# Kernel tuning notes

Hardware: AMD Instinct MI355X
Metric: run time of the kernel (lower is better)

The kernel has to match this reference:

```python
import jax, jax.numpy as jnp
import numpy as np

D = 256; R = 2; K = 32
N = 32768; NE = 1_000_000; NT = 65_536
BETA_MAX = 5.0; GRAD_CLIP = 1.0; STATE_CLIP = 10.0
DAMP = 0.9999  # update_damping=1.0 clamped to 1-1e-4
EPS = 1e-5


def _xavier(key, din, dout, gain=0.5):
    lim = gain * np.sqrt(6.0 / (din + dout))
    return jax.random.uniform(key, (din, dout), jnp.float32, -lim, lim)


def setup_inputs() -> dict:
    key = jax.random.key(0)
    ks = jax.random.split(key, 16)
    inv_sp1 = float(np.log(np.expm1(1.0)))  # inverse softplus of 1.0
    return {
        "X": jax.random.normal(ks[0], (N, D), jnp.float32),
        "c_2": jax.random.randint(ks[1], (NE,), 0, N, jnp.int32),
        "u_2": jax.random.randint(ks[2], (NE,), 0, N, jnp.int32),
        "c_3": jax.random.randint(ks[3], (NT,), 0, N, jnp.int32),
        "u_3": jax.random.randint(ks[4], (NT,), 0, N, jnp.int32),
        "v_3": jax.random.randint(ks[5], (NT,), 0, N, jnp.int32),
        "t_tau": jax.random.randint(ks[6], (NT,), 0, 2, jnp.int32),
        "step_size": jnp.float32(0.1),
        "ln_gamma": jnp.ones((D,), jnp.float32),
        "ln_beta": jnp.zeros((D,), jnp.float32),
        "W_Q2": _xavier(ks[7], D, D),
        "W_K2": _xavier(ks[8], D, D),
        "W_Q3": _xavier(ks[9], D, R * D),
        "W_K3": _xavier(ks[10], D, R * D),
        "T_tau": 0.02 * jax.random.normal(ks[11], (2, R, D), jnp.float32),
        "W_Qm": _xavier(ks[12], D, D),
        "W_Km": _xavier(ks[13], D, D),
        "B_mem": jax.random.normal(ks[14], (K, D), jnp.float32) / np.sqrt(D),
        "lambda_2": jnp.float32(inv_sp1), "lambda_3": jnp.float32(inv_sp1), "lambda_m": jnp.float32(inv_sp1),
        "beta_2": jnp.float32(inv_sp1), "beta_3": jnp.float32(inv_sp1), "beta_m": jnp.float32(inv_sp1),
    }


def _seg_lse(s, seg, n):
    # logsumexp of s grouped by seg; empty segments contribute 0
    m = jax.ops.segment_max(s, seg, num_segments=n)
    m0 = jnp.where(jnp.isfinite(m), m, 0.0)
    e = jax.ops.segment_sum(jnp.exp(s - m0[seg]), seg, num_segments=n)
    return jnp.where(e > 0, m0 + jnp.log(jnp.maximum(e, 1e-30)), 0.0)


def _energy(X, ln_gamma, ln_beta, W_Q2, W_K2, W_Q3, W_K3, T_tau, W_Qm, W_Km, B_mem,
            lambda_2, lambda_3, lambda_m, beta_2, beta_3, beta_m,
            c_2, u_2, c_3, u_3, v_3, t_tau):
    mu = X.mean(-1, keepdims=True)
    var = ((X - mu) ** 2).mean(-1, keepdims=True)
    G = (X - mu) * jax.lax.rsqrt(var + EPS) * ln_gamma + ln_beta  # [N,D]
    sp = jax.nn.softplus
    lam2, lam3, lamm = sp(lambda_2), sp(lambda_3), sp(lambda_m)
    b2 = jnp.minimum(sp(beta_2), BETA_MAX)
    b3 = jnp.minimum(sp(beta_3), BETA_MAX)
    bm = jnp.minimum(sp(beta_m), BETA_MAX)
    scale = jnp.float32(1.0 / np.sqrt(D))
    # pairwise (order-2) attention energy over edge list
    Q2, K2 = G @ W_Q2, G @ W_K2
    s2 = b2 * scale * jnp.sum(Q2[c_2] * K2[u_2], axis=-1)  # [NE]
    E2 = -(lam2 / b2) * jnp.sum(_seg_lse(s2, c_2, N))
    # motif (order-3) rank-R energy over triangle list with type embedding T_tau
    Q3 = (G @ W_Q3).reshape(N, R, D)
    K3 = (G @ W_K3).reshape(N, R, D)
    s3 = b3 * scale * jnp.sum(Q3[c_3] * K3[u_3] * K3[v_3] * T_tau[t_tau], axis=(1, 2))  # [NT]
    E3 = -(lam3 / b3) * jnp.sum(_seg_lse(s3, c_3, N))
    # memory-slot energy
    Qm, Km = G @ W_Qm, B_mem @ W_Km  # [N,D],[K,D]
    Sm = bm * scale * (Qm @ Km.T)  # [N,K]
    Em = -(lamm / bm) * jnp.sum(jax.nn.logsumexp(Sm, axis=-1))
    return E2 + E3 + Em


def reference(X, c_2, u_2, c_3, u_3, v_3, t_tau, step_size, ln_gamma, ln_beta,
              W_Q2, W_K2, W_Q3, W_K3, T_tau, W_Qm, W_Km, B_mem,
              lambda_2, lambda_3, lambda_m, beta_2, beta_3, beta_m):
    efn = lambda x: _energy(x, ln_gamma, ln_beta, W_Q2, W_K2, W_Q3, W_K3, T_tau,
                            W_Qm, W_Km, B_mem, lambda_2, lambda_3, lambda_m,
                            beta_2, beta_3, beta_m, c_2, u_2, c_3, u_3, v_3, t_tau)
    E, gX = jax.value_and_grad(efn)(X)
    gn = jnp.maximum(jnp.linalg.norm(gX, axis=-1, keepdims=True), 1e-6)
    gX = gX * jnp.minimum(GRAD_CLIP / gn, 1.0)
    X_next = X - step_size * DAMP * gX
    sn = jnp.maximum(jnp.linalg.norm(X_next, axis=-1, keepdims=True), 1e-6)
    X_next = X_next * jnp.minimum(STATE_CLIP / sn, 1.0)
    return X_next, E
```

## Files before the change

kernel.cpp:

```cpp
#include <hip/hip_runtime.h>
#include <math.h>

#define D_ 256
#define KSLOT 32
#define CAP2 128
#define CAP3C 16
#define CAP3I 32
#define NBP 256
#define NBUCK 256
typedef unsigned short ushort_t;
typedef __attribute__((ext_vector_type(8))) short bf16x8;
typedef __attribute__((ext_vector_type(4))) float f32x4;

__device__ __forceinline__ float softplus_f(float x){
  return (x > 20.0f) ? x : log1pf(expf(x));
}
__device__ __forceinline__ float bflo(unsigned u){ return __uint_as_float(u << 16); }
__device__ __forceinline__ float bfhi(unsigned u){ return __uint_as_float(u & 0xFFFF0000u); }
__device__ __forceinline__ ushort_t f2b(float f){
  unsigned u = __float_as_uint(f);
  unsigned r = u + 0x7FFFu + ((u >> 16) & 1u);
  return (ushort_t)(r >> 16);
}
__device__ __forceinline__ unsigned pack2(float a, float b){
  return (unsigned)f2b(a) | ((unsigned)f2b(b) << 16);
}
__device__ __forceinline__ void unpack16(uint4 a, uint4 b, float* f){
  f[0]=bflo(a.x); f[1]=bfhi(a.x); f[2]=bflo(a.y); f[3]=bfhi(a.y);
  f[4]=bflo(a.z); f[5]=bfhi(a.z); f[6]=bflo(a.w); f[7]=bfhi(a.w);
  f[8]=bflo(b.x); f[9]=bfhi(b.x); f[10]=bflo(b.y); f[11]=bfhi(b.y);
  f[12]=bflo(b.z); f[13]=bfhi(b.z); f[14]=bflo(b.w); f[15]=bfhi(b.w);
}
__device__ __forceinline__ float block_reduce_sum(float v, float* sbuf){
  #pragma unroll
  for (int o = 32; o > 0; o >>= 1) v += __shfl_xor(v, o);
  int t = threadIdx.x, wid = t >> 6, lane = t & 63;
  if (lane == 0) sbuf[wid] = v;
  __syncthreads();
  if (t == 0) sbuf[0] = sbuf[0] + sbuf[1] + sbuf[2] + sbuf[3];
  __syncthreads();
  float r = sbuf[0];
  __syncthreads();
  return r;
}

__global__ __launch_bounds__(256) void zerok(float4* __restrict__ p, size_t n4){
  float4 z; z.x = z.y = z.z = z.w = 0.f;
  for (size_t i = (size_t)blockIdx.x * 256 + threadIdx.x; i < n4; i += (size_t)gridDim.x * 256)
    p[i] = z;
}

__global__ __launch_bounds__(256) void ln_fwd(const float* __restrict__ X, const float* __restrict__ gamma,
    const float* __restrict__ beta, ushort_t* __restrict__ Gb, float* __restrict__ mean, float* __restrict__ rstd)
{
  __shared__ float sbuf[8];
  int n = blockIdx.x, t = threadIdx.x;
  size_t idx = (size_t)n * D_ + t;
  float x = X[idx];
  float mu = block_reduce_sum(x, sbuf) * (1.0f / D_);
  float d = x - mu;
  float var = block_reduce_sum(d * d, sbuf) * (1.0f / D_);
  float rs = rsqrtf(var + 1e-5f);
  Gb[idx] = f2b(d * rs * gamma[t] + beta[t]);
  if (t == 0){ mean[n] = mu; rstd[n] = rs; }
}

__global__ __launch_bounds__(256) void wprep_all(const float* __restrict__ W_Q2, const float* __restrict__ W_K2,
    const float* __restrict__ W_Q3, const float* __restrict__ W_K3, const float* __restrict__ W_Qm,
    ushort_t* __restrict__ WtQm, ushort_t* __restrict__ WtF2, ushort_t* __restrict__ WtF3,
    ushort_t* __restrict__ WbQm, ushort_t* __restrict__ Bt2, ushort_t* __restrict__ Bt3)
{
  int idx = blockIdx.x * 256 + threadIdx.x;
  if (idx < 65536){
    int m = idx >> 8, k = idx & 255;
    WtQm[idx] = f2b(W_Qm[k * 256 + m]);
    return;
  }
  idx -= 65536;
  if (idx < 131072){
    int m = idx >> 8, k = idx & 255;
    WtF2[idx] = f2b(m < 256 ? W_Q2[k * 256 + m] : W_K2[k * 256 + (m - 256)]);
    return;
  }
  idx -= 131072;
  if (idx < 262144){
    int m = idx >> 8, k = idx & 255;
    WtF3[idx] = f2b(m < 512 ? W_Q3[k * 512 + m] : W_K3[k * 512 + (m - 512)]);
    return;
  }
  idx -= 262144;
  if (idx < 65536){ WbQm[idx] = f2b(W_Qm[idx]); return; }
  idx -= 65536;
  if (idx < 131072){
    int d = idx >> 9, k = idx & 511;
    Bt2[idx] = f2b(k < 256 ? W_Q2[d * 256 + k] : W_K2[d * 256 + (k - 256)]);
    return;
  }
  idx -= 131072;
  if (idx < 262144){
    int d = idx >> 10, k = idx & 1023;
    Bt3[idx] = f2b(k < 512 ? W_Q3[d * 512 + k] : W_K3[d * 512 + (k - 512)]);
  }
}

template<int OUT_MODE>
__global__ __launch_bounds__(256) void gemm_bt_mfma(const ushort_t* __restrict__ A,
    const ushort_t* __restrict__ Bt, void* __restrict__ C, int K, int M)
{
  __shared__ __align__(16) ushort_t As[128 * 32];
  __shared__ __align__(16) ushort_t Bs[128 * 32];
  int t = threadIdx.x;
  int wave = t >> 6, lane = t & 63;
  int row0 = blockIdx.y * 128;
  int col0 = blockIdx.x * 128;
  int wrow = (wave & 1) * 64;
  int wcol = (wave >> 1) * 64;
  f32x4 acc[4][4];
  #pragma unroll
  for (int i = 0; i < 4; ++i)
    #pragma unroll
    for (int j = 0; j < 4; ++j)
      acc[i][j] = (f32x4){0.f, 0.f, 0.f, 0.f};
  int srow = wave * 32 + (lane >> 2);
  int skoff = (lane & 3) * 8;
  const ushort_t* Ag0 = A + (size_t)(row0 + srow) * K + skoff;
  const ushort_t* Ag1 = A + (size_t)(row0 + srow + 16) * K + skoff;
  const ushort_t* Bg0 = Bt + (size_t)(col0 + srow) * K + skoff;
  const ushort_t* Bg1 = Bt + (size_t)(col0 + srow + 16) * K + skoff;
  ushort_t* Al0 = As + wave * 1024;
  ushort_t* Al1 = As + wave * 1024 + 512;
  ushort_t* Bl0 = Bs + wave * 1024;
  ushort_t* Bl1 = Bs + wave * 1024 + 512;
  int lrow = lane & 15, lk = (lane >> 4) * 8;
  for (int k0 = 0; k0 < K; k0 += 32){
    __syncthreads();
    __builtin_amdgcn_global_load_lds((const __attribute__((address_space(1))) void*)(Ag0 + k0),
                                     (__attribute__((address_space(3))) void*)Al0, 16, 0, 0);
    __builtin_amdgcn_global_load_lds((const __attribute__((address_space(1))) void*)(Ag1 + k0),
                                     (__attribute__((address_space(3))) void*)Al1, 16, 0, 0);
    __builtin_amdgcn_global_load_lds((const __attribute__((address_space(1))) void*)(Bg0 + k0),
                                     (__attribute__((address_space(3))) void*)Bl0, 16, 0, 0);
    __builtin_amdgcn_global_load_lds((const __attribute__((address_space(1))) void*)(Bg1 + k0),
                                     (__attribute__((address_space(3))) void*)Bl1, 16, 0, 0);
    __syncthreads();
    bf16x8 af[4], bf_[4];
    #pragma unroll
    for (int i = 0; i < 4; ++i)
      af[i] = *(const bf16x8*)(As + (wrow + i * 16 + lrow) * 32 + lk);
    #pragma unroll
    for (int j = 0; j < 4; ++j)
      bf_[j] = *(const bf16x8*)(Bs + (wcol + j * 16 + lrow) * 32 + lk);
    #pragma unroll
    for (int i = 0; i < 4; ++i)
      #pragma unroll
      for (int j = 0; j < 4; ++j)
        acc[i][j] = __builtin_amdgcn_mfma_f32_16x16x32_bf16(af[i], bf_[j], acc[i][j], 0, 0, 0);
  }
  int rbase = row0 + wrow + (lane >> 4) * 4;
  int cbase = col0 + wcol + (lane & 15);
  #pragma unroll
  for (int i = 0; i < 4; ++i){
    #pragma unroll
    for (int r = 0; r < 4; ++r){
      size_t rowoff = (size_t)(rbase + i * 16 + r) * M;
      #pragma unroll
      for (int j = 0; j < 4; ++j){
        int col = cbase + j * 16;
        float v = acc[i][j][r];
        if (OUT_MODE == 0)      ((float*)C)[rowoff + col] = v;
        else if (OUT_MODE == 1) ((float*)C)[rowoff + col] += v;
        else                    ((ushort_t*)C)[rowoff + col] = f2b(v);
      }
    }
  }
}

__global__ __launch_bounds__(256) void km_kernel(const float* __restrict__ Bm, const float* __restrict__ W,
    ushort_t* __restrict__ Kmb)
{
  __shared__ float sb[D_];
  int k = blockIdx.x, t = threadIdx.x;
  if (k < KSLOT){
    sb[t] = Bm[(size_t)k * D_ + t];
    __syncthreads();
    float acc = 0.f;
    for (int d = 0; d < D_; ++d) acc += sb[d] * W[(size_t)d * D_ + t];
    Kmb[(size_t)k * D_ + t] = f2b(acc);
  } else {
    Kmb[(size_t)k * D_ + t] = 0;
  }
}

__global__ __launch_bounds__(256) void softmax32(const float* __restrict__ Sm, ushort_t* __restrict__ Pb,
    float* __restrict__ lseM, const float* __restrict__ bmp, const float* __restrict__ lmp)
{
  int t = threadIdx.x;
  int r = blockIdx.x * 8 + (t >> 5);
  int lane = t & 31;
  float bs = fminf(softplus_f(*bmp), 5.0f) * 0.0625f;
  float coef = -softplus_f(*lmp) * 0.0625f;
  float s = Sm[(size_t)r * 128 + lane] * bs;
  float m = s;
  #pragma unroll
  for (int o = 16; o > 0; o >>= 1) m = fmaxf(m, __shfl_xor(m, o, 32));
  float e = __expf(s - m);
  float se = e;
  #pragma unroll
  for (int o = 16; o > 0; o >>= 1) se += __shfl_xor(se, o, 32);
  ushort_t* dst = Pb + (size_t)r * 128 + lane;
  dst[0] = f2b(coef * e / se);
  dst[32] = 0; dst[64] = 0; dst[96] = 0;
  if (lane == 0) lseM[r] = m + logf(se);
}

__global__ __launch_bounds__(256) void p2_hist(const unsigned* __restrict__ key, int stride, int NE_, int chunk,
    unsigned* __restrict__ bh)
{
  __shared__ unsigned h[256];
  int t = threadIdx.x, b = blockIdx.x;
  h[t] = 0;
  __syncthreads();
  int s = b * chunk, e = s + chunk; if (e > NE_) e = NE_;
  for (int i = s + t; i < e; i += 256)
    atomicAdd(&h[(key[(size_t)i * stride] >> 7) & 255u], 1u);
  __syncthreads();
  bh[b * 256 + t] = h[t];
}

__global__ __launch_bounds__(256) void p2_scan(unsigned* __restrict__ bh, int nb, unsigned* __restrict__ base)
{
  __shared__ unsigned ss[256];
  int t = threadIdx.x;
  unsigned tot = 0;
  for (int b = 0; b < nb; ++b) tot += bh[b * 256 + t];
  ss[t] = tot;
  __syncthreads();
  #pragma unroll
  for (int o = 1; o < 256; o <<= 1){
    unsigned v = (t >= o) ? ss[t - o] : 0u;
    __syncthreads();
    ss[t] += v;
    __syncthreads();
  }
  unsigned excl = ss[t] - tot;
  base[t] = excl;
  if (t == 255) base[256] = ss[t];
  unsigned run = excl;
  for (int b = 0; b < nb; ++b){
    unsigned v = bh[b * 256 + t];
    bh[b * 256 + t] = run;
    run += v;
  }
}

__global__ __launch_bounds__(256) void p2_place_c(const int* __restrict__ c2, const int* __restrict__ u2,
    int NE_, int chunk, const unsigned* __restrict__ bh, unsigned* __restrict__ part)
{
  __shared__ unsigned cur[256];
  int t = threadIdx.x, b = blockIdx.x;
  cur[t] = bh[b * 256 + t];
  __syncthreads();
  int s = b * chunk, e = s + chunk; if (e > NE_) e = NE_;
  for (int i = s + t; i < e; i += 256){
    unsigned c = (unsigned)c2[i], u = (unsigned)u2[i];
    unsigned dst = atomicAdd(&cur[c >> 7], 1u);
    part[dst] = ((c & 127u) << 15) | u;
  }
}

__global__ __launch_bounds__(256) void p2_fine_c(const unsigned* __restrict__ part, const unsigned* __restrict__ base,
    ushort_t* __restrict__ adjc, int* __restrict__ cntC, uint2* __restrict__ pairsU)
{
  __shared__ unsigned cnt[128];
  __shared__ ushort_t stage[128 * 128];
  int t = threadIdx.x, b = blockIdx.x;
  if (t < 128) cnt[t] = 0;
  __syncthreads();
  int s = (int)base[b], e = (int)base[b + 1];
  for (int i = s + t; i < e; i += 256){
    unsigned w = part[i];
    unsigned r = w >> 15, u = w & 32767u;
    unsigned slot = atomicAdd(&cnt[r], 1u);
    uint2 pr;
    pr.x = u;
    if (slot < 128u){
      stage[r * 128 + slot] = (ushort_t)u;
      pr.y = (((unsigned)b * 128u + r) << 7) | slot;
    } else {
      pr.y = 0xFFFFFFFFu;
    }
    pairsU[i] = pr;
  }
  __syncthreads();
  if (t < 128) cntC[b * 128 + t] = (int)cnt[t];
  for (int i = t; i < 16384; i += 256)
    adjc[(size_t)b * 16384 + i] = stage[i];
}

__global__ __launch_bounds__(256) void p2_place_u(const uint2* __restrict__ pairs, int NE_, int chunk,
    const unsigned* __restrict__ bh, uint2* __restrict__ part)
{
  __shared__ unsigned cur[256];
  int t = threadIdx.x, b = blockIdx.x;
  cur[t] = bh[b * 256 + t];
  __syncthreads();
  int s = b * chunk, e = s + chunk; if (e > NE_) e = NE_;
  for (int i = s + t; i < e; i += 256){
    uint2 pr = pairs[i];
    unsigned dst = atomicAdd(&cur[pr.x >> 7], 1u);
    part[dst] = pr;
  }
}

__global__ __launch_bounds__(256) void p2_fine_u(const uint2* __restrict__ part, const unsigned* __restrict__ base,
    int* __restrict__ adju, int* __restrict__ cntU)
{
  __shared__ unsigned cnt[128];
  __shared__ unsigned stage[128 * 128];
  int t = threadIdx.x, b = blockIdx.x;
  if (t < 128) cnt[t] = 0;
  __syncthreads();
  int s = (int)base[b], e = (int)base[b + 1];
  for (int i = s + t; i < e; i += 256){
    uint2 pr = part[i];
    if (pr.y == 0xFFFFFFFFu) continue;
    unsigned r = pr.x & 127u;
    unsigned slot = atomicAdd(&cnt[r], 1u);
    if (slot < 128u) stage[r * 128 + slot] = pr.y;
  }
  __syncthreads();
  if (t < 128) cntU[b * 128 + t] = (int)cnt[t];
  for (int i = t; i < 16384; i += 256)
    adju[(size_t)b * 16384 + i] = (int)stage[i];
}

__global__ __launch_bounds__(256) void scatter3(const int* __restrict__ c3, const int* __restrict__ u3,
    const int* __restrict__ v3, const int* __restrict__ tt, int* __restrict__ cnt3C, int* __restrict__ cnt3I,
    unsigned* __restrict__ adj3c, uint2* __restrict__ adj3i, int NT_)
{
  int e = blockIdx.x * 256 + threadIdx.x;
  if (e >= NT_) return;
  int c = c3[e], u = u3[e], v = v3[e], tau = tt[e];
  int pc = atomicAdd(cnt3C + c, 1);
  if (pc >= CAP3C) return;
  int cslot = (c << 4) + pc;
  adj3c[cslot] = (unsigned)u | ((unsigned)v << 15) | ((unsigned)tau << 30);
  int pu = atomicAdd(cnt3I + u, 1);
  if (pu < CAP3I){
    uint2 eu; eu.x = (unsigned)c | ((unsigned)tau << 15) | ((unsigned)v << 16); eu.y = (unsigned)cslot;
    adj3i[(u << 5) + pu] = eu;
  }
  int pv = atomicAdd(cnt3I + v, 1);
  if (pv < CAP3I){
    uint2 ev; ev.x = (unsigned)c | ((unsigned)tau << 15) | ((unsigned)u << 16); ev.y = (unsigned)cslot;
    adj3i[(v << 5) + pv] = ev;
  }
}

__global__ __launch_bounds__(256) void e2_rowc(const ushort_t* __restrict__ QK2, const int* __restrict__ cntC,
    const ushort_t* __restrict__ adjc, ushort_t* __restrict__ dstage, float* __restrict__ s2e,
    float2* __restrict__ ml2, const float* __restrict__ b2p, const float* __restrict__ l2p)
{
  int wave = threadIdx.x >> 6, lane = threadIdx.x & 63;
  int r = blockIdx.x * 4 + wave;
  int quarter = lane >> 4, sub = lane & 15;
  float b2s = fminf(softplus_f(*b2p), 5.0f) * 0.0625f;
  float lam2 = softplus_f(*l2p);
  int start = r << 7;
  int deg = cntC[r]; if (deg > CAP2) deg = CAP2;
  int end = start + deg;
  unsigned subo = (unsigned)sub * 16u;
  const ushort_t* qrow = QK2 + ((unsigned)r << 9) + subo;
  float qf[16];
  unpack16(*(const uint4*)qrow, *(const uint4*)(qrow + 8), qf);
  #pragma unroll
  for (int j = 0; j < 16; ++j) qf[j] *= b2s;
  float l = 0.f;
  float a[16] = {};
  int p = start + quarter;
  uint4 k0, k1;
  if (p < end){
    unsigned off = ((unsigned)adjc[p] << 9) + 256u + subo;
    k0 = *(const uint4*)(QK2 + off); k1 = *(const uint4*)(QK2 + off + 8);
  }
  while (p < end){
    int pn = p + 4;
    uint4 n0, n1;
    if (pn < end){
      unsigned off = ((unsigned)adjc[pn] << 9) + 256u + subo;
      n0 = *(const uint4*)(QK2 + off); n1 = *(const uint4*)(QK2 + off + 8);
    }
    float kf[16];
    unpack16(k0, k1, kf);
    float d = 0.f;
    #pragma unroll
    for (int j = 0; j < 16; ++j) d += qf[j] * kf[j];
    d += __shfl_xor(d, 1); d += __shfl_xor(d, 2); d += __shfl_xor(d, 4); d += __shfl_xor(d, 8);
    float pt = __expf(d);
    if (sub == 0) s2e[p] = pt;
    l += pt;
    #pragma unroll
    for (int j = 0; j < 16; ++j) a[j] += pt * kf[j];
    k0 = n0; k1 = n1; p = pn;
  }
  float L = l;
  L += __shfl_xor(L, 16); L += __shfl_xor(L, 32);
  #pragma unroll
  for (int j = 0; j < 16; ++j){
    float x = a[j];
    x += __shfl_xor(x, 16); x += __shfl_xor(x, 32);
    a[j] = x;
  }
  float linv = 0.f, coef = 0.f;
  if (deg > 0){ linv = 1.0f / L; coef = -lam2 * 0.0625f * linv; }
  if (lane == 0){
    float2 ml; ml.x = 0.f; ml.y = linv;
    ml2[r] = ml;
  }
  if (quarter == 0){
    ushort_t* dst = dstage + ((unsigned)r << 9) + subo;
    uint4 p0, p1;
    p0.x = pack2(coef*a[0], coef*a[1]);   p0.y = pack2(coef*a[2], coef*a[3]);
    p0.z = pack2(coef*a[4], coef*a[5]);   p0.w = pack2(coef*a[6], coef*a[7]);
    p1.x = pack2(coef*a[8], coef*a[9]);   p1.y = pack2(coef*a[10], coef*a[11]);
    p1.z = pack2(coef*a[12], coef*a[13]); p1.w = pack2(coef*a[14], coef*a[15]);
    *(uint4*)dst = p0; *(uint4*)(dst + 8) = p1;
  }
}

__global__ __launch_bounds__(256) void e2_rowu(const ushort_t* __restrict__ QK2, const int* __restrict__ cntU,
    const int* __restrict__ adju, const float* __restrict__ s2e, const float2* __restrict__ ml2,
    ushort_t* __restrict__ dstage, const float* __restrict__ l2p)
{
  int wave = threadIdx.x >> 6, lane = threadIdx.x & 63;
  int r = blockIdx.x * 4 + wave;
  int quarter = lane >> 4, sub = lane & 15;
  float lam2 = softplus_f(*l2p);
  int start = r << 7;
  int deg = cntU[r]; if (deg > CAP2) deg = CAP2;
  int end = start + deg;
  unsigned subo = (unsigned)sub * 16u;
  float a[16] = {};
  int p = start + quarter;
  uint4 q0a, q0b; float sv0 = 0.f; float2 mlv0 = {0.f, 0.f};
  if (p < end){
    unsigned gs = (unsigned)adju[p];
    unsigned c = gs >> 7;
    sv0 = s2e[gs]; mlv0 = ml2[c];
    unsigned off = (c << 9) + subo;
    q0a = *(const uint4*)(QK2 + off); q0b = *(const uint4*)(QK2 + off + 8);
  }
  while (p < end){
    int pn = p + 4;
    uint4 q1a, q1b; float sv1 = 0.f; float2 mlv1 = {0.f, 0.f};
    if (pn < end){
      unsigned gs = (unsigned)adju[pn];
      unsigned c = gs >> 7;
      sv1 = s2e[gs]; mlv1 = ml2[c];
      unsigned off = (c << 9) + subo;
      q1a = *(const uint4*)(QK2 + off); q1b = *(const uint4*)(QK2 + off + 8);
    }
    float pe = sv0 * mlv0.y;
    float qf[16];
    unpack16(q0a, q0b, qf);
    #pragma unroll
    for (int j = 0; j < 16; ++j) a[j] += pe * qf[j];
    q0a = q1a; q0b = q1b; sv0 = sv1; mlv0 = mlv1; p = pn;
  }
  #pragma unroll
  for (int j = 0; j < 16; ++j){
    float x = a[j];
    x += __shfl_xor(x, 16); x += __shfl_xor(x, 32);
    a[j] = x;
  }
  float coef = -lam2 * 0.0625f;
  if (quarter == 0){
    ushort_t* dst = dstage + ((unsigned)r << 9) + 256u + subo;
    uint4 p0, p1;
    p0.x = pack2(coef*a[0], coef*a[1]);   p0.y = pack2(coef*a[2], coef*a[3]);
    p0.z = pack2(coef*a[4], coef*a[5]);   p0.w = pack2(coef*a[6], coef*a[7]);
    p1.x = pack2(coef*a[8], coef*a[9]);   p1.y = pack2(coef*a[10], coef*a[11]);
    p1.z = pack2(coef*a[12], coef*a[13]); p1.w = pack2(coef*a[14], coef*a[15]);
    *(uint4*)dst = p0; *(uint4*)(dst + 8) = p1;
  }
}

__global__ __launch_bounds__(256) void e3_rowc(const ushort_t* __restrict__ QK3, const float* __restrict__ Tt,
    const int* __restrict__ cnt3C, const unsigned* __restrict__ adj3c, ushort_t* __restrict__ dstage,
    float* __restrict__ s3c, float2* __restrict__ ml3, const float* __restrict__ b3p,
    const float* __restrict__ l3p)
{
  __shared__ float sT[1024];
  int wave = threadIdx.x >> 6, lane = threadIdx.x & 63;
  int r = blockIdx.x * 4 + wave;
  for (int i = threadIdx.x; i < 1024; i += 256) sT[i] = Tt[i];
  __syncthreads();
  float b3s = fminf(softplus_f(*b3p), 5.0f) * 0.0625f;
  float lam3 = softplus_f(*l3p);
  int start = r << 4;
  int deg = cnt3C[r]; if (deg > CAP3C) deg = CAP3C;
  int end = start + deg;
  unsigned laneo = (unsigned)lane * 8u;
  uint4 qw = *(const uint4*)(QK3 + ((unsigned)r << 10) + laneo);
  float q[8] = {bflo(qw.x),bfhi(qw.x),bflo(qw.y),bfhi(qw.y),bflo(qw.z),bfhi(qw.z),bflo(qw.w),bfhi(qw.w)};
  #pragma unroll
  for (int j = 0; j < 8; ++j) q[j] *= b3s;
  float T0[8], T1[8];
  #pragma unroll
  for (int j = 0; j < 8; ++j){ T0[j] = sT[lane * 8 + j]; T1[j] = sT[512 + lane * 8 + j]; }
  float l = 0.f;
  float a[8] = {};
  int p = start;
  unsigned ent0 = 0; uint4 bw0, cw0;
  if (p < end){
    ent0 = adj3c[p];
    unsigned u = ent0 & 32767u, v = (ent0 >> 15) & 32767u;
    bw0 = *(const uint4*)(QK3 + (u << 10) + 512u + laneo);
    cw0 = *(const uint4*)(QK3 + (v << 10) + 512u + laneo);
  }
  while (p < end){
    int pn = p + 1;
    unsigned ent1 = 0; uint4 bw1, cw1;
    if (pn < end){
      ent1 = adj3c[pn];
      unsigned u = ent1 & 32767u, v = (ent1 >> 15) & 32767u;
      bw1 = *(const uint4*)(QK3 + (u << 10) + 512u + laneo);
      cw1 = *(const uint4*)(QK3 + (v << 10) + 512u + laneo);
    }
    int tau = (ent0 >> 30) & 1;
    float kb[8] = {bflo(bw0.x),bfhi(bw0.x),bflo(bw0.y),bfhi(bw0.y),bflo(bw0.z),bfhi(bw0.z),bflo(bw0.w),bfhi(bw0.w)};
    float kc[8] = {bflo(cw0.x),bfhi(cw0.x),bflo(cw0.y),bfhi(cw0.y),bflo(cw0.z),bfhi(cw0.z),bflo(cw0.w),bfhi(cw0.w)};
    float prod[8];
    float d = 0.f;
    #pragma unroll
    for (int j = 0; j < 8; ++j){
      float tj = tau ? T1[j] : T0[j];
      prod[j] = kb[j] * kc[j] * tj;
      d += q[j] * prod[j];
    }
    #pragma unroll
    for (int o = 32; o > 0; o >>= 1) d += __shfl_xor(d, o);
    float pt = __expf(d);
    if (lane == 0) s3c[p] = pt;
    l += pt;
    #pragma unroll
    for (int j = 0; j < 8; ++j) a[j] += pt * prod[j];
    ent0 = ent1; bw0 = bw1; cw0 = cw1; p = pn;
  }
  float linv = 0.f, coef = 0.f;
  if (deg > 0){ linv = 1.0f / l; coef = -lam3 * 0.0625f * linv; }
  uint4 o4;
  o4.x = pack2(coef*a[0], coef*a[1]); o4.y = pack2(coef*a[2], coef*a[3]);
  o4.z = pack2(coef*a[4], coef*a[5]); o4.w = pack2(coef*a[6], coef*a[7]);
  *(uint4*)(dstage + ((unsigned)r << 10) + laneo) = o4;
  if (lane == 0){
    float2 ml; ml.x = 0.f; ml.y = linv;
    ml3[r] = ml;
  }
}

__global__ __launch_bounds__(256) void e3_rowi(const ushort_t* __restrict__ QK3, const float* __restrict__ Tt,
    const int* __restrict__ cnt3I, const uint2* __restrict__ adj3i, const float* __restrict__ s3c,
    const float2* __restrict__ ml3, ushort_t* __restrict__ dstage, const float* __restrict__ l3p)
{
  __shared__ float sT[1024];
  int wave = threadIdx.x >> 6, lane = threadIdx.x & 63;
  int r = blockIdx.x * 4 + wave;
  for (int i = threadIdx.x; i < 1024; i += 256) sT[i] = Tt[i];
  __syncthreads();
  float lam3 = softplus_f(*l3p);
  int start = r << 5;
  int deg = cnt3I[r]; if (deg > CAP3I) deg = CAP3I;
  int end = start + deg;
  unsigned laneo = (unsigned)lane * 8u;
  float T0[8], T1[8];
  #pragma unroll
  for (int j = 0; j < 8; ++j){ T0[j] = sT[lane * 8 + j]; T1[j] = sT[512 + lane * 8 + j]; }
  float a[8] = {};
  int p = start;
  uint2 e0; uint4 qw0, ow0; float sv0 = 0.f; float2 mlv0 = {0.f, 0.f};
  if (p < end){
    e0 = adj3i[p];
    unsigned c = e0.x & 32767u, other = (e0.x >> 16) & 32767u;
    sv0 = s3c[e0.y]; mlv0 = ml3[c];
    qw0 = *(const uint4*)(QK3 + (c << 10) + laneo);
    ow0 = *(const uint4*)(QK3 + (other << 10) + 512u + laneo);
  }
  while (p < end){
    int pn = p + 1;
    uint2 e1; uint4 qw1, ow1; float sv1 = 0.f; float2 mlv1 = {0.f, 0.f};
    if (pn < end){
      e1 = adj3i[pn];
      unsigned c = e1.x & 32767u, other = (e1.x >> 16) & 32767u;
      sv1 = s3c[e1.y]; mlv1 = ml3[c];
      qw1 = *(const uint4*)(QK3 + (c << 10) + laneo);
      ow1 = *(const uint4*)(QK3 + (other << 10) + 512u + laneo);
    }
    int tau = (e0.x >> 15) & 1;
    float pe = sv0 * mlv0.y;
    float q[8] = {bflo(qw0.x),bfhi(qw0.x),bflo(qw0.y),bfhi(qw0.y),bflo(qw0.z),bfhi(qw0.z),bflo(qw0.w),bfhi(qw0.w)};
    float ko[8] = {bflo(ow0.x),bfhi(ow0.x),bflo(ow0.y),bfhi(ow0.y),bflo(ow0.z),bfhi(ow0.z),bflo(ow0.w),bfhi(ow0.w)};
    #pragma unroll
    for (int j = 0; j < 8; ++j){
      float tj = tau ? T1[j] : T0[j];
      a[j] += pe * q[j] * ko[j] * tj;
    }
    e0 = e1; qw0 = qw1; ow0 = ow1; sv0 = sv1; mlv0 = mlv1; p = pn;
  }
  float coef = -lam3 * 0.0625f;
  uint4 o4;
  o4.x = pack2(coef*a[0], coef*a[1]); o4.y = pack2(coef*a[2], coef*a[3]);
  o4.z = pack2(coef*a[4], coef*a[5]); o4.w = pack2(coef*a[6], coef*a[7]);
  *(uint4*)(dstage + ((unsigned)r << 10) + 512u + laneo) = o4;
}

__global__ __launch_bounds__(256) void ln_bwd_update(const float* __restrict__ X, const float* __restrict__ dG,
    const float* __restrict__ gamma, const float* __restrict__ mean, const float* __restrict__ rstd,
    const float* __restrict__ step_p, float* __restrict__ out)
{
  __shared__ float sbuf[8];
  int n = blockIdx.x, t = threadIdx.x;
  size_t idx = (size_t)n * D_ + t;
  float x = X[idx];
  float rs = rstd[n];
  float xh = (x - mean[n]) * rs;
  float dxh = dG[idx] * gamma[t];
  float s1 = block_reduce_sum(dxh, sbuf) * (1.0f / D_);
  float s2v = block_reduce_sum(dxh * xh, sbuf) * (1.0f / D_);
  float dx = rs * (dxh - s1 - xh * s2v);
  float gn2 = block_reduce_sum(dx * dx, sbuf);
  float gn = fmaxf(sqrtf(gn2), 1e-6f);
  float gsc = fminf(1.0f / gn, 1.0f);
  float stp = step_p[0] * 0.9999f;
  float xn = x - stp * gsc * dx;
  float sn2 = block_reduce_sum(xn * xn, sbuf);
  float sn = fmaxf(sqrtf(sn2), 1e-6f);
  float ssc = fminf(10.0f / sn, 1.0f);
  out[idx] = xn * ssc;
}

__global__ __launch_bounds__(256) void energy_partial(const float2* __restrict__ ml2, const float2* __restrict__ ml3,
    const float* __restrict__ lseM, int n, float* __restrict__ eacc)
{
  __shared__ float sbuf[8];
  int t = threadIdx.x;
  float a2 = 0.f, a3 = 0.f, am = 0.f;
  for (int i = blockIdx.x * 256 + t; i < n; i += gridDim.x * 256){
    float2 v2 = ml2[i];
    if (v2.y > 0.f) a2 += v2.x - logf(v2.y);
    float2 v3 = ml3[i];
    if (v3.y > 0.f) a3 += v3.x - logf(v3.y);
    am += lseM[i];
  }
  float s2 = block_reduce_sum(a2, sbuf);
  float s3 = block_reduce_sum(a3, sbuf);
  float sm = block_reduce_sum(am, sbuf);
  if (t == 0){
    atomicAdd(eacc + 0, s2);
    atomicAdd(eacc + 1, s3);
    atomicAdd(eacc + 2, sm);
  }
}

__global__ __launch_bounds__(64) void energy_combine(const float* __restrict__ eacc,
    const float* l2p, const float* l3p, const float* lmp,
    const float* b2p, const float* b3p, const float* bmp, float* __restrict__ outE)
{
  if (threadIdx.x == 0){
    float l2 = softplus_f(*l2p), l3 = softplus_f(*l3p), lm = softplus_f(*lmp);
    float b2 = fminf(softplus_f(*b2p), 5.0f);
    float b3 = fminf(softplus_f(*b3p), 5.0f);
    float bm = fminf(softplus_f(*bmp), 5.0f);
    *outE = -(l2 / b2) * eacc[0] - (l3 / b3) * eacc[1] - (lm / bm) * eacc[2];
  }
}

static inline void zfill(void* p, size_t nElems, hipStream_t stream){
  size_t n4 = nElems / 4;
  int blocks = (int)(((n4 + 255) / 256) < 16384 ? ((n4 + 255) / 256) : 16384);
  if (blocks < 1) blocks = 1;
  zerok<<<blocks, 256, 0, stream>>>((float4*)p, n4);
}

extern "C" void kernel_launch(void* const* d_in, const int* in_sizes, int n_in,
                              void* d_out, int out_size, void* d_ws, size_t ws_size,
                              hipStream_t stream)
{
  const float* X     = (const float*)d_in[0];
  const int*   c2    = (const int*)d_in[1];
  const int*   u2    = (const int*)d_in[2];
  const int*   c3    = (const int*)d_in[3];
  const int*   u3    = (const int*)d_in[4];
  const int*   v3    = (const int*)d_in[5];
  const int*   tt    = (const int*)d_in[6];
  const float* stepp = (const float*)d_in[7];
  const float* gamma = (const float*)d_in[8];
  const float* beta  = (const float*)d_in[9];
  const float* W_Q2  = (const float*)d_in[10];
  const float* W_K2  = (const float*)d_in[11];
  const float* W_Q3  = (const float*)d_in[12];
  const float* W_K3  = (const float*)d_in[13];
  const float* T_tau = (const float*)d_in[14];
  const float* W_Qm  = (const float*)d_in[15];
  const float* W_Km  = (const float*)d_in[16];
  const float* B_mem = (const float*)d_in[17];
  const float* l2p   = (const float*)d_in[18];
  const float* l3p   = (const float*)d_in[19];
  const float* lmp   = (const float*)d_in[20];
  const float* b2p   = (const float*)d_in[21];
  const float* b3p   = (const float*)d_in[22];
  const float* bmp   = (const float*)d_in[23];

  const int N  = in_sizes[0] / D_;
  const int NE = in_sizes[1];
  const int NT = in_sizes[3];
  const size_t ND = (size_t)N * D_;

  char* base = (char*)d_ws;
  size_t off = 0;
  auto alloc = [&](size_t bytes) -> void* {
    void* p = base + off;
    off += (bytes + 255) & ~(size_t)255;
    return p;
  };
  ushort_t* Gb    = (ushort_t*)alloc(ND * 2);
  ushort_t* bufA  = (ushort_t*)alloc(ND * 4 * 2);
  ushort_t* bufB  = (ushort_t*)alloc(ND * 4 * 2);
  int*      zreg  = (int*)     alloc(((size_t)4 * N + 16) * 4);
  ushort_t* adjc  = (ushort_t*)alloc((size_t)N * CAP2 * 2);
  int*      adju  = (int*)     alloc((size_t)N * CAP2 * 4);
  unsigned* adj3c = (unsigned*)alloc((size_t)N * CAP3C * 4);
  uint2*    adj3i = (uint2*)   alloc((size_t)N * CAP3I * 8);
  float*    s3c   = (float*)   alloc((size_t)N * CAP3C * 4);
  float2*   ml2   = (float2*)  alloc((size_t)N * 8);
  float2*   ml3   = (float2*)  alloc((size_t)N * 8);
  ushort_t* Kmb   = (ushort_t*)alloc((size_t)128 * 256 * 2);
  ushort_t* KWb   = (ushort_t*)alloc((size_t)256 * 128 * 2);
  float*    meanb = (float*)   alloc((size_t)N * 4);
  float*    rstdb = (float*)   alloc((size_t)N * 4);
  float*    lseM  = (float*)   alloc((size_t)N * 4);
  ushort_t* WtQm  = (ushort_t*)alloc(65536 * 2);
  ushort_t* WtF2  = (ushort_t*)alloc(131072 * 2);
  ushort_t* WtF3  = (ushort_t*)alloc(262144 * 2);
  ushort_t* WbQm  = (ushort_t*)alloc(65536 * 2);
  ushort_t* Bt2   = (ushort_t*)alloc(131072 * 2);
  ushort_t* Bt3   = (ushort_t*)alloc(262144 * 2);

  int* cntC  = zreg;
  int* cntU  = zreg + N;
  int* cnt3C = zreg + 2 * N;
  int* cnt3I = zreg + 3 * N;
  float* eacc = (float*)(zreg + 4 * N);
  float* out = (float*)d_out;
  float*    Sm  = (float*)bufB;
  ushort_t* Pb  = (ushort_t*)(Sm + (size_t)N * 128);
  float*    s2e = (float*)(bufB + ND * 2);

  unsigned* partA  = (unsigned*)bufA;
  uint2*    pairsU = (uint2*)((char*)bufA + ((size_t)8 << 20));
  unsigned* bhC    = (unsigned*)((char*)bufA + ((size_t)16 << 20));
  unsigned* bhU    = bhC + NBP * 256;
  unsigned* baseC  = bhU + NBP * 256;
  unsigned* baseU  = baseC + 512;

  zfill(zreg, (size_t)4 * N + 16, stream);

  ln_fwd<<<N, 256, 0, stream>>>(X, gamma, beta, Gb, meanb, rstdb);
  wprep_all<<<(917504 + 255) / 256, 256, 0, stream>>>(W_Q2, W_K2, W_Q3, W_K3, W_Qm,
      WtQm, WtF2, WtF3, WbQm, Bt2, Bt3);

  {
    int chunk = (NE + NBP - 1) / NBP;
    p2_hist<<<NBP, 256, 0, stream>>>((const unsigned*)c2, 1, NE, chunk, bhC);
    p2_scan<<<1, 256, 0, stream>>>(bhC, NBP, baseC);
    p2_place_c<<<NBP, 256, 0, stream>>>(c2, u2, NE, chunk, bhC, partA);
    p2_fine_c<<<NBUCK, 256, 0, stream>>>(partA, baseC, adjc, cntC, pairsU);
    p2_hist<<<NBP, 256, 0, stream>>>((const unsigned*)pairsU, 2, NE, chunk, bhU);
    p2_scan<<<1, 256, 0, stream>>>(bhU, NBP, baseU);
    p2_place_u<<<NBP, 256, 0, stream>>>(pairsU, NE, chunk, bhU, (uint2*)partA);
    p2_fine_u<<<NBUCK, 256, 0, stream>>>((const uint2*)partA, baseU, adju, cntU);
  }
  scatter3<<<(NT + 255) / 256, 256, 0, stream>>>(c3, u3, v3, tt, cnt3C, cnt3I, adj3c, adj3i, NT);

  dim3 g256(2, N / 128), g512(4, N / 128), g1024(8, N / 128);

  km_kernel<<<128, 256, 0, stream>>>(B_mem, W_Km, Kmb);
  gemm_bt_mfma<2><<<dim3(1, 2), 256, 0, stream>>>(WbQm, Kmb, KWb, 256, 128);
  gemm_bt_mfma<2><<<g256, 256, 0, stream>>>(Gb, WtQm, bufA, D_, D_);
  gemm_bt_mfma<0><<<dim3(1, N / 128), 256, 0, stream>>>(bufA, Kmb, Sm, 256, 128);
  softmax32<<<N / 8, 256, 0, stream>>>(Sm, Pb, lseM, bmp, lmp);
  gemm_bt_mfma<0><<<g256, 256, 0, stream>>>(Pb, KWb, out, 128, D_);

  gemm_bt_mfma<2><<<g512, 256, 0, stream>>>(Gb, WtF2, bufA, D_, 512);
  e2_rowc<<<N / 4, 256, 0, stream>>>(bufA, cntC, adjc, bufB, s2e, ml2, b2p, l2p);
  e2_rowu<<<N / 4, 256, 0, stream>>>(bufA, cntU, adju, s2e, ml2, bufB, l2p);
  gemm_bt_mfma<1><<<g256, 256, 0, stream>>>(bufB, Bt2, out, 512, D_);

  gemm_bt_mfma<2><<<g1024, 256, 0, stream>>>(Gb, WtF3, bufA, D_, 1024);
  e3_rowc<<<N / 4, 256, 0, stream>>>(bufA, T_tau, cnt3C, adj3c, bufB, s3c, ml3, b3p, l3p);
  e3_rowi<<<N / 4, 256, 0, stream>>>(bufA, T_tau, cnt3I, adj3i, s3c, ml3, bufB, l3p);
  gemm_bt_mfma<1><<<g256, 256, 0, stream>>>(bufB, Bt3, out, 1024, D_);

  ln_bwd_update<<<N, 256, 0, stream>>>(X, out, gamma, meanb, rstdb, stepp, out);

  energy_partial<<<128, 256, 0, stream>>>(ml2, ml3, lseM, N, eacc);
  energy_combine<<<1, 64, 0, stream>>>(eacc, l2p, l3p, lmp, b2p, b3p, bmp, out + ND);
}
```

Measured before the change: 827.5 us.

## Swizzle GEMM LDS layout and pre-normalize edge scores before scatter passes

Result: no change. 830.5 us (+0.4%).

```diff
diff --git a/kernel.cpp b/kernel.cpp
--- a/kernel.cpp
+++ b/kernel.cpp
@@ -122,7 +122,7 @@
     for (int j = 0; j < 4; ++j)
       acc[i][j] = (f32x4){0.f, 0.f, 0.f, 0.f};
   int srow = wave * 32 + (lane >> 2);
-  int skoff = (lane & 3) * 8;
+  int skoff = (((lane & 3) ^ ((lane >> 3) & 3))) * 8;
   const ushort_t* Ag0 = A + (size_t)(row0 + srow) * K + skoff;
   const ushort_t* Ag1 = A + (size_t)(row0 + srow + 16) * K + skoff;
   const ushort_t* Bg0 = Bt + (size_t)(col0 + srow) * K + skoff;
@@ -132,6 +132,7 @@
   ushort_t* Bl0 = Bs + wave * 1024;
   ushort_t* Bl1 = Bs + wave * 1024 + 512;
   int lrow = lane & 15, lk = (lane >> 4) * 8;
+  int lkx = lk ^ (((lrow >> 1) & 3) * 8);
   for (int k0 = 0; k0 < K; k0 += 32){
     __syncthreads();
     __builtin_amdgcn_global_load_lds((const __attribute__((address_space(1))) void*)(Ag0 + k0),
@@ -146,10 +147,10 @@
     bf16x8 af[4], bf_[4];
     #pragma unroll
     for (int i = 0; i < 4; ++i)
-      af[i] = *(const bf16x8*)(As + (wrow + i * 16 + lrow) * 32 + lk);
+      af[i] = *(const bf16x8*)(As + (wrow + i * 16 + lrow) * 32 + lkx);
     #pragma unroll
     for (int j = 0; j < 4; ++j)
-      bf_[j] = *(const bf16x8*)(Bs + (wcol + j * 16 + lrow) * 32 + lk);
+      bf_[j] = *(const bf16x8*)(Bs + (wcol + j * 16 + lrow) * 32 + lkx);
     #pragma unroll
     for (int i = 0; i < 4; ++i)
       #pragma unroll
@@ -357,6 +358,17 @@
   }
 }
 
+__global__ __launch_bounds__(256) void pnorm(float4* __restrict__ s, const float2* __restrict__ ml,
+    int shift, int n4)
+{
+  int i = blockIdx.x * 256 + threadIdx.x;
+  if (i >= n4) return;
+  float linv = ml[(unsigned)(i << 2) >> shift].y;
+  float4 v = s[i];
+  v.x *= linv; v.y *= linv; v.z *= linv; v.w *= linv;
+  s[i] = v;
+}
+
 __global__ __launch_bounds__(256) void e2_rowc(const ushort_t* __restrict__ QK2, const int* __restrict__ cntC,
     const ushort_t* __restrict__ adjc, ushort_t* __restrict__ dstage, float* __restrict__ s2e,
     float2* __restrict__ ml2, const float* __restrict__ b2p, const float* __restrict__ l2p)
@@ -429,7 +441,7 @@
 }
 
 __global__ __launch_bounds__(256) void e2_rowu(const ushort_t* __restrict__ QK2, const int* __restrict__ cntU,
-    const int* __restrict__ adju, const float* __restrict__ s2e, const float2* __restrict__ ml2,
+    const int* __restrict__ adju, const float* __restrict__ s2e,
     ushort_t* __restrict__ dstage, const float* __restrict__ l2p)
 {
   int wave = threadIdx.x >> 6, lane = threadIdx.x & 63;
@@ -442,30 +454,27 @@
   unsigned subo = (unsigned)sub * 16u;
   float a[16] = {};
   int p = start + quarter;
-  uint4 q0a, q0b; float sv0 = 0.f; float2 mlv0 = {0.f, 0.f};
+  uint4 q0a, q0b; float pe0 = 0.f;
   if (p < end){
     unsigned gs = (unsigned)adju[p];
-    unsigned c = gs >> 7;
-    sv0 = s2e[gs]; mlv0 = ml2[c];
-    unsigned off = (c << 9) + subo;
+    pe0 = s2e[gs];
+    unsigned off = ((gs >> 7) << 9) + subo;
     q0a = *(const uint4*)(QK2 + off); q0b = *(const uint4*)(QK2 + off + 8);
   }
   while (p < end){
     int pn = p + 4;
-    uint4 q1a, q1b; float sv1 = 0.f; float2 mlv1 = {0.f, 0.f};
+    uint4 q1a, q1b; float pe1 = 0.f;
     if (pn < end){
       unsigned gs = (unsigned)adju[pn];
-      unsigned c = gs >> 7;
-      sv1 = s2e[gs]; mlv1 = ml2[c];
-      unsigned off = (c << 9) + subo;
+      pe1 = s2e[gs];
+      unsigned off = ((gs >> 7) << 9) + subo;
       q1a = *(const uint4*)(QK2 + off); q1b = *(const uint4*)(QK2 + off + 8);
     }
-    float pe = sv0 * mlv0.y;
     float qf[16];
     unpack16(q0a, q0b, qf);
     #pragma unroll
-    for (int j = 0; j < 16; ++j) a[j] += pe * qf[j];
-    q0a = q1a; q0b = q1b; sv0 = sv1; mlv0 = mlv1; p = pn;
+    for (int j = 0; j < 16; ++j) a[j] += pe0 * qf[j];
+    q0a = q1a; q0b = q1b; pe0 = pe1; p = pn;
   }
   #pragma unroll
   for (int j = 0; j < 16; ++j){
@@ -561,7 +570,7 @@
 
 __global__ __launch_bounds__(256) void e3_rowi(const ushort_t* __restrict__ QK3, const float* __restrict__ Tt,
     const int* __restrict__ cnt3I, const uint2* __restrict__ adj3i, const float* __restrict__ s3c,
-    const float2* __restrict__ ml3, ushort_t* __restrict__ dstage, const float* __restrict__ l3p)
+    ushort_t* __restrict__ dstage, const float* __restrict__ l3p)
 {
   __shared__ float sT[1024];
   int wave = threadIdx.x >> 6, lane = threadIdx.x & 63;
@@ -578,34 +587,33 @@
   for (int j = 0; j < 8; ++j){ T0[j] = sT[lane * 8 + j]; T1[j] = sT[512 + lane * 8 + j]; }
   float a[8] = {};
   int p = start;
-  uint2 e0; uint4 qw0, ow0; float sv0 = 0.f; float2 mlv0 = {0.f, 0.f};
+  uint2 e0; uint4 qw0, ow0; float pe0 = 0.f;
   if (p < end){
     e0 = adj3i[p];
     unsigned c = e0.x & 32767u, other = (e0.x >> 16) & 32767u;
-    sv0 = s3c[e0.y]; mlv0 = ml3[c];
+    pe0 = s3c[e0.y];
     qw0 = *(const uint4*)(QK3 + (c << 10) + laneo);
     ow0 = *(const uint4*)(QK3 + (other << 10) + 512u + laneo);
   }
   while (p < end){
     int pn = p + 1;
-    uint2 e1; uint4 qw1, ow1; float sv1 = 0.f; float2 mlv1 = {0.f, 0.f};
+    uint2 e1; uint4 qw1, ow1; float pe1 = 0.f;
     if (pn < end){
       e1 = adj3i[pn];
       unsigned c = e1.x & 32767u, other = (e1.x >> 16) & 32767u;
-      sv1 = s3c[e1.y]; mlv1 = ml3[c];
+      pe1 = s3c[e1.y];
       qw1 = *(const uint4*)(QK3 + (c << 10) + laneo);
       ow1 = *(const uint4*)(QK3 + (other << 10) + 512u + laneo);
     }
     int tau = (e0.x >> 15) & 1;
-    float pe = sv0 * mlv0.y;
     float q[8] = {bflo(qw0.x),bfhi(qw0.x),bflo(qw0.y),bfhi(qw0.y),bflo(qw0.z),bfhi(qw0.z),bflo(qw0.w),bfhi(qw0.w)};
     float ko[8] = {bflo(ow0.x),bfhi(ow0.x),bflo(ow0.y),bfhi(ow0.y),bflo(ow0.z),bfhi(ow0.z),bflo(ow0.w),bfhi(ow0.w)};
     #pragma unroll
     for (int j = 0; j < 8; ++j){
       float tj = tau ? T1[j] : T0[j];
-      a[j] += pe * q[j] * ko[j] * tj;
+      a[j] += pe0 * q[j] * ko[j] * tj;
     }
-    e0 = e1; qw0 = qw1; ow0 = ow1; sv0 = sv1; mlv0 = mlv1; p = pn;
+    e0 = e1; qw0 = qw1; ow0 = ow1; pe0 = pe1; p = pn;
   }
   float coef = -lam3 * 0.0625f;
   uint4 o4;
@@ -793,12 +801,14 @@
 
   gemm_bt_mfma<2><<<g512, 256, 0, stream>>>(Gb, WtF2, bufA, D_, 512);
   e2_rowc<<<N / 4, 256, 0, stream>>>(bufA, cntC, adjc, bufB, s2e, ml2, b2p, l2p);
-  e2_rowu<<<N / 4, 256, 0, stream>>>(bufA, cntU, adju, s2e, ml2, bufB, l2p);
+  pnorm<<<(N * CAP2 / 4 + 255) / 256, 256, 0, stream>>>((float4*)s2e, ml2, 7, N * CAP2 / 4);
+  e2_rowu<<<N / 4, 256, 0, stream>>>(bufA, cntU, adju, s2e, bufB, l2p);
   gemm_bt_mfma<1><<<g256, 256, 0, stream>>>(bufB, Bt2, out, 512, D_);
 
   gemm_bt_mfma<2><<<g1024, 256, 0, stream>>>(Gb, WtF3, bufA, D_, 1024);
   e3_rowc<<<N / 4, 256, 0, stream>>>(bufA, T_tau, cnt3C, adj3c, bufB, s3c, ml3, b3p, l3p);
-  e3_rowi<<<N / 4, 256, 0, stream>>>(bufA, T_tau, cnt3I, adj3i, s3c, ml3, bufB, l3p);
+  pnorm<<<(N * CAP3C / 4 + 255) / 256, 256, 0, stream>>>((float4*)s3c, ml3, 4, N * CAP3C / 4);
+  e3_rowi<<<N / 4, 256, 0, stream>>>(bufA, T_tau, cnt3I, adj3i, s3c, bufB, l3p);
   gemm_bt_mfma<1><<<g256, 256, 0, stream>>>(bufB, Bt3, out, 1024, D_);
 
   ln_bwd_update<<<N, 256, 0, stream>>>(X, out, gamma, meanb, rstdb, stepp, out);
```
